# Kernel optimization log

Measured on AMD Instinct MI355X. Metric: run time of the kernel, lower is better.

The kernel has to match this reference:

```python
import jax, jax.numpy as jnp
import numpy as np

B, N, C = 16, 4096, 1024
H = 8          # heads
K_DIM = 1024   # k_dim from init
DH = C // H    # per-head dim = 128


def setup_inputs() -> dict:
    key = jax.random.key(0)
    k1, k2, k3, k4 = jax.random.split(key, 4)
    x = jax.random.normal(k1, (B, N, C), dtype=jnp.float32)
    # torch Linear weight is [out,in]; we store [in,out] so y = x @ W
    Wq = jax.random.normal(k2, (DH, K_DIM // H), dtype=jnp.float32) * (1.0 / np.sqrt(DH))
    Wk = jax.random.normal(k3, (DH, K_DIM // H), dtype=jnp.float32) * (1.0 / np.sqrt(DH))
    Wv = jax.random.normal(k4, (DH, DH), dtype=jnp.float32) * (1.0 / np.sqrt(DH))
    return {"x": x, "Wq": Wq, "Wk": Wk, "Wv": Wv}


def reference(x, Wq, Wk, Wv):
    b, n, c = x.shape
    xh = x.reshape(b, n, H, c // H)              # [B,N,H,dh]
    q = jnp.einsum('bnhd,de->bnhe', xh, Wq)      # [B,N,H,dk]
    k = jnp.einsum('bnhd,de->bnhe', xh, Wk)
    v = jnp.einsum('bnhd,de->bnhe', xh, Wv)
    # NB: attention is across the HEAD axis (matmul over last two dims of [B,N,H,d])
    scale = H / K_DIM
    aff = jnp.einsum('bnhe,bnge->bnhg', q, k) * scale   # [B,N,H,H]
    attn = jax.nn.softmax(aff, axis=-1)
    ctx = jnp.einsum('bnhg,bngd->bnhd', attn, v)        # [B,N,H,dv]
    return ctx.reshape(b, n, -1)
```

## Files before the change

kernel.cpp:

```cpp
#include <hip/hip_runtime.h>
#include <hip/hip_bf16.h>


typedef short s16x8 __attribute__((ext_vector_type(8)));
typedef float f32x4 __attribute__((ext_vector_type(4)));

#define NHEAD 8
#define DHEAD 128
#define TB 8
#define MROWS 64
#define QK_STRIDE 136
#define VT_STRIDE 80

__device__ __forceinline__ short f2bf(float f) {
    union { __hip_bfloat16 h; short s; } u;
    u.h = __float2bfloat16(f);
    return u.s;
}

__global__ __launch_bounds__(256, 2)
void fused_head_attn(const float* __restrict__ x,
                     const float* __restrict__ Wq,
                     const float* __restrict__ Wk,
                     const float* __restrict__ Wv,
                     float* __restrict__ out)
{
    __shared__ short q_s[MROWS * QK_STRIDE];
    __shared__ short k_s[MROWS * QK_STRIDE];
    __shared__ short v_t[DHEAD * VT_STRIDE];

    const int tid  = threadIdx.x;
    const int wave = tid >> 6;
    const int lane = tid & 63;
    const int lr   = lane & 15;
    const int lq   = lane >> 4;

    const long tok_base = (long)blockIdx.x * TB;
    const float* x_tile = x + tok_base * 1024;

    {
        int r = tid >> 1, half = tid & 1;
        *reinterpret_cast<int4*>(&v_t[r * VT_STRIDE + 64 + half * 8]) =
            make_int4(0, 0, 0, 0);
    }

    s16x8 afrag[4][4];
    #pragma unroll
    for (int m = 0; m < 4; ++m) {
        #pragma unroll
        for (int kk = 0; kk < 4; ++kk) {
            const float* p = x_tile + (m * 16 + lr) * 128 + kk * 32 + lq * 8;
            float4 u0 = *reinterpret_cast<const float4*>(p);
            float4 u1 = *reinterpret_cast<const float4*>(p + 4);
            s16x8 a;
            a[0] = f2bf(u0.x); a[1] = f2bf(u0.y); a[2] = f2bf(u0.z); a[3] = f2bf(u0.w);
            a[4] = f2bf(u1.x); a[5] = f2bf(u1.y); a[6] = f2bf(u1.z); a[7] = f2bf(u1.w);
            afrag[m][kk] = a;
        }
    }

    const int colbase = wave * 32;
    const float* Ws[3] = {Wq, Wk, Wv};
    #pragma unroll
    for (int mat = 0; mat < 3; ++mat) {
        const float* W = Ws[mat];
        s16x8 bfrag[2][4];
        #pragma unroll
        for (int n = 0; n < 2; ++n) {
            int col = colbase + n * 16 + lr;
            #pragma unroll
            for (int kk = 0; kk < 4; ++kk) {
                int k0 = kk * 32 + lq * 8;
                s16x8 b;
                #pragma unroll
                for (int j = 0; j < 8; ++j)
                    b[j] = f2bf(W[(k0 + j) * 128 + col]);
                bfrag[n][kk] = b;
            }
        }
        #pragma unroll
        for (int m = 0; m < 4; ++m) {
            #pragma unroll
            for (int n = 0; n < 2; ++n) {
                f32x4 acc = {0.f, 0.f, 0.f, 0.f};
                #pragma unroll
                for (int kk = 0; kk < 4; ++kk)
                    acc = __builtin_amdgcn_mfma_f32_16x16x32_bf16(
                        afrag[m][kk], bfrag[n][kk], acc, 0, 0, 0);
                const int col   = colbase + n * 16 + lr;
                const int rbase = m * 16 + lq * 4;
                if (mat == 0) {
                    #pragma unroll
                    for (int r = 0; r < 4; ++r)
                        q_s[(rbase + r) * QK_STRIDE + col] = f2bf(acc[r]);
                } else if (mat == 1) {
                    #pragma unroll
                    for (int r = 0; r < 4; ++r)
                        k_s[(rbase + r) * QK_STRIDE + col] = f2bf(acc[r]);
                } else {
                    short4 pk;
                    pk.x = f2bf(acc[0]); pk.y = f2bf(acc[1]);
                    pk.z = f2bf(acc[2]); pk.w = f2bf(acc[3]);
                    *reinterpret_cast<short4*>(&v_t[col * VT_STRIDE + rbase]) = pk;
                }
            }
        }
    }

    __syncthreads();

    const int rb = wave * 16;

    s16x8 qf[4], kf[4];
    #pragma unroll
    for (int kk = 0; kk < 4; ++kk) {
        qf[kk] = *reinterpret_cast<const s16x8*>(
            &q_s[(rb + lr) * QK_STRIDE + kk * 32 + lq * 8]);
        kf[kk] = *reinterpret_cast<const s16x8*>(
            &k_s[(rb + lr) * QK_STRIDE + kk * 32 + lq * 8]);
    }
    f32x4 aff = {0.f, 0.f, 0.f, 0.f};
    #pragma unroll
    for (int kk = 0; kk < 4; ++kk)
        aff = __builtin_amdgcn_mfma_f32_16x16x32_bf16(qf[kk], kf[kk], aff, 0, 0, 0);

    const float scale = 0.0078125f;
    const bool valid  = (lr < 8) == (lq < 2);
    float p[4];
    #pragma unroll
    for (int r = 0; r < 4; ++r) {
        float s0 = aff[r] * scale;
        float mx = s0;
        mx = fmaxf(mx, __shfl_xor(mx, 1));
        mx = fmaxf(mx, __shfl_xor(mx, 2));
        mx = fmaxf(mx, __shfl_xor(mx, 4));
        float e = __expf(s0 - mx);
        float sum = e;
        sum += __shfl_xor(sum, 1);
        sum += __shfl_xor(sum, 2);
        sum += __shfl_xor(sum, 4);
        p[r] = valid ? (e / sum) : 0.f;
    }

    if (lane < 32) {
        *reinterpret_cast<int4*>(&q_s[(rb + lr) * QK_STRIDE + 16 + lq * 8]) =
            make_int4(0, 0, 0, 0);
    }
    {
        const int rbase = rb + lq * 4;
        #pragma unroll
        for (int r = 0; r < 4; ++r)
            q_s[(rbase + r) * QK_STRIDE + lr] = f2bf(p[r]);
    }
    asm volatile("s_waitcnt lgkmcnt(0)" ::: "memory");
    __builtin_amdgcn_sched_barrier(0);

    s16x8 pa = *reinterpret_cast<const s16x8*>(&q_s[(rb + lr) * QK_STRIDE + lq * 8]);

    float* out_tile = out + tok_base * 1024 + (long)wave * 2048;
    #pragma unroll
    for (int nf = 0; nf < 8; ++nf) {
        s16x8 bv = *reinterpret_cast<const s16x8*>(
            &v_t[(nf * 16 + lr) * VT_STRIDE + rb + lq * 8]);
        f32x4 c = {0.f, 0.f, 0.f, 0.f};
        c = __builtin_amdgcn_mfma_f32_16x16x32_bf16(pa, bv, c, 0, 0, 0);
        #pragma unroll
        for (int r = 0; r < 4; ++r)
            out_tile[(lq * 4 + r) * 128 + nf * 16 + lr] = c[r];
    }
}

extern "C" void kernel_launch(void* const* d_in, const int* in_sizes, int n_in,
                              void* d_out, int out_size, void* d_ws, size_t ws_size,
                              hipStream_t stream) {
    const float* x  = (const float*)d_in[0];
    const float* Wq = (const float*)d_in[1];
    const float* Wk = (const float*)d_in[2];
    const float* Wv = (const float*)d_in[3];
    float* outp = (float*)d_out;

    const int tokens = 16 * 4096;
    dim3 grid(tokens / TB), block(256);
    fused_head_attn<<<grid, block, 0, stream>>>(x, Wq, Wk, Wv, outp);
}
```

Baseline: 566.8 us.

## Pre-convert weights to transposed bf16 and shrink V tile stride

Adds a small pre-kernel that converts Wq/Wk/Wv to bf16 in a transposed [col][k] layout in workspace. The main kernel then loads each B fragment as one 16-byte vector instead of eight strided fp32 loads plus conversions in every block. The V transpose buffer stride shrinks and its zero-padding is dropped; the P·V B-operand instead reuses the lower 8 rows for the upper k-half, which P's zeros mask out. Occupancy hint rises to 3 blocks per SM. This adds an extra kernel launch and depends on the workspace being large enough.

```diff
diff --git a/kernel.cpp b/kernel.cpp
--- a/kernel.cpp
+++ b/kernel.cpp
@@ -10,7 +10,7 @@
 #define TB 8
 #define MROWS 64
 #define QK_STRIDE 136
-#define VT_STRIDE 80
+#define VT_STRIDE 72
 
 __device__ __forceinline__ short f2bf(float f) {
     union { __hip_bfloat16 h; short s; } u;
@@ -18,11 +18,23 @@
     return u.s;
 }
 
-__global__ __launch_bounds__(256, 2)
+__global__ void conv_weights(const float* __restrict__ Wq,
+                             const float* __restrict__ Wk,
+                             const float* __restrict__ Wv,
+                             short* __restrict__ wt)
+{
+    int i = blockIdx.x * 256 + threadIdx.x;
+    int mat = i >> 14;
+    int r   = i & 16383;
+    int c   = r >> 7;
+    int k   = r & 127;
+    const float* W = (mat == 0) ? Wq : ((mat == 1) ? Wk : Wv);
+    wt[i] = f2bf(W[k * 128 + c]);
+}
+
+__global__ __launch_bounds__(256, 3)
 void fused_head_attn(const float* __restrict__ x,
-                     const float* __restrict__ Wq,
-                     const float* __restrict__ Wk,
-                     const float* __restrict__ Wv,
+                     const short* __restrict__ wt,
                      float* __restrict__ out)
 {
     __shared__ short q_s[MROWS * QK_STRIDE];
@@ -37,12 +49,6 @@
 
     const long tok_base = (long)blockIdx.x * TB;
     const float* x_tile = x + tok_base * 1024;
-
-    {
-        int r = tid >> 1, half = tid & 1;
-        *reinterpret_cast<int4*>(&v_t[r * VT_STRIDE + 64 + half * 8]) =
-            make_int4(0, 0, 0, 0);
-    }
 
     s16x8 afrag[4][4];
     #pragma unroll
@@ -60,23 +66,17 @@
     }
 
     const int colbase = wave * 32;
-    const float* Ws[3] = {Wq, Wk, Wv};
     #pragma unroll
     for (int mat = 0; mat < 3; ++mat) {
-        const float* W = Ws[mat];
+        const short* Wt = wt + mat * 16384;
         s16x8 bfrag[2][4];
         #pragma unroll
         for (int n = 0; n < 2; ++n) {
             int col = colbase + n * 16 + lr;
             #pragma unroll
-            for (int kk = 0; kk < 4; ++kk) {
-                int k0 = kk * 32 + lq * 8;
-                s16x8 b;
-                #pragma unroll
-                for (int j = 0; j < 8; ++j)
-                    b[j] = f2bf(W[(k0 + j) * 128 + col]);
-                bfrag[n][kk] = b;
-            }
+            for (int kk = 0; kk < 4; ++kk)
+                bfrag[n][kk] = *reinterpret_cast<const s16x8*>(
+                    Wt + col * 128 + kk * 32 + lq * 8);
         }
         #pragma unroll
         for (int m = 0; m < 4; ++m) {
@@ -157,11 +157,12 @@
 
     s16x8 pa = *reinterpret_cast<const s16x8*>(&q_s[(rb + lr) * QK_STRIDE + lq * 8]);
 
+    const int vk = rb + (lq & 1) * 8;
     float* out_tile = out + tok_base * 1024 + (long)wave * 2048;
     #pragma unroll
     for (int nf = 0; nf < 8; ++nf) {
         s16x8 bv = *reinterpret_cast<const s16x8*>(
-            &v_t[(nf * 16 + lr) * VT_STRIDE + rb + lq * 8]);
+            &v_t[(nf * 16 + lr) * VT_STRIDE + vk]);
         f32x4 c = {0.f, 0.f, 0.f, 0.f};
         c = __builtin_amdgcn_mfma_f32_16x16x32_bf16(pa, bv, c, 0, 0, 0);
         #pragma unroll
@@ -178,8 +179,11 @@
     const float* Wk = (const float*)d_in[2];
     const float* Wv = (const float*)d_in[3];
     float* outp = (float*)d_out;
+    short* wt   = (short*)d_ws;
+
+    conv_weights<<<dim3(192), dim3(256), 0, stream>>>(Wq, Wk, Wv, wt);
 
     const int tokens = 16 * 4096;
     dim3 grid(tokens / TB), block(256);
-    fused_head_attn<<<grid, block, 0, stream>>>(x, Wq, Wk, Wv, outp);
+    fused_head_attn<<<grid, block, 0, stream>>>(x, wt, outp);
 }
```

After: 540.3 us. 4.7% less time.
